# Performance work log

Measured on AMD Instinct MI355X. Metric: run time of the kernel, lower is better.

The kernel has to match this reference:

```python
import jax, jax.numpy as jnp
import numpy as np

D_MODEL = 2816
N_EXPERTS = 64
TOP_K = 8
RMS_EPS = 1e-6


def setup_inputs() -> dict:
    key = jax.random.key(0)
    k1, k2, k3, k4 = jax.random.split(key, 4)
    x = jax.random.normal(k1, (8, 4096, D_MODEL), dtype=jnp.float32)
    W = jax.random.normal(k2, (N_EXPERTS, D_MODEL), dtype=jnp.float32) * (D_MODEL ** -0.5)
    scale = jax.random.uniform(k3, (D_MODEL,), dtype=jnp.float32)
    per_expert_scale = jax.random.uniform(k4, (N_EXPERTS,), dtype=jnp.float32)
    return {"x": x, "W": W, "scale": scale, "per_expert_scale": per_expert_scale}


def reference(x, W, scale, per_expert_scale):
    # RMSNorm (no learned scale in norm itself)
    v = jnp.mean(jnp.square(x), axis=-1, keepdims=True)
    h = x * jax.lax.rsqrt(v + RMS_EPS)
    # elementwise scale + 1/sqrt(d)
    h = h * scale * (D_MODEL ** -0.5)
    # tiny projection to expert logits: [B,S,E]
    scores = jnp.einsum('bsd,ed->bse', h, W)
    prob = jax.nn.softmax(scores, axis=-1)
    topw, topi = jax.lax.top_k(prob, TOP_K)          # [B,S,K]
    topw = topw / jnp.sum(topw, axis=-1, keepdims=True)
    topw = topw * per_expert_scale[topi]
    # one-hot scatter back to dense [B,S,E]
    oh = jax.nn.one_hot(topi, N_EXPERTS, dtype=topw.dtype)  # [B,S,K,E]
    return jnp.einsum('bsk,bske->bse', topw, oh)
```

## Files before the change

kernel.cpp:

```cpp
#include <hip/hip_runtime.h>
#include <math.h>

#define D_MODEL 2816
#define N_EXP   64
#define TOPK    8
#define T_TILE  64
#define DC      32
#define NCHUNK  88
#define SROW    34
#define SMEM_BYTES 35072


__global__ __launch_bounds__(256, 2)
void router_fused(const float* __restrict__ x,
                  const float* __restrict__ W,
                  const float* __restrict__ scale,
                  const float* __restrict__ pes,
                  float* __restrict__ out)
{
    __shared__ __align__(16) char smem[SMEM_BYTES];
    double (*xs)[SROW] = (double (*)[SROW])(smem);
    double (*ws)[SROW] = (double (*)[SROW])(smem + 64 * SROW * 8);
    double* raw  = (double*)smem;
    float*  ssqp = (float*)(smem + 32768);
    float*  rn   = (float*)(smem + 34816);

    const int tid  = threadIdx.x;
    const int tb   = blockIdx.x * T_TILE;
    const int lrow = tid >> 3;
    const int kk   = tid & 7;
    const int tg4  = (tid >> 4) << 2;
    const int eg   = tid & 15;

    double acc[4][4] = {};
    float ssq2[2] = {0.f, 0.f};

    for (int c = 0; c < NCHUNK; ++c) {
        const int d0 = c * DC;
        float4 xg[2], wg[2];
        const float4 sc4 = *(const float4*)(scale + d0 + kk * 4);
        #pragma unroll
        for (int r = 0; r < 2; ++r) {
            const int row = r * 32 + lrow;
            xg[r] = *(const float4*)(x + (size_t)(tb + row) * D_MODEL + d0 + kk * 4);
            wg[r] = *(const float4*)(W + (size_t)row * D_MODEL + d0 + kk * 4);
        }
        __syncthreads();
        #pragma unroll
        for (int r = 0; r < 2; ++r) {
            const int row = r * 32 + lrow;
            ssq2[r] += xg[r].x * xg[r].x + xg[r].y * xg[r].y
                     + xg[r].z * xg[r].z + xg[r].w * xg[r].w;
            double2* xrow = (double2*)&xs[row][kk * 4];
            xrow[0] = make_double2((double)xg[r].x, (double)xg[r].y);
            xrow[1] = make_double2((double)xg[r].z, (double)xg[r].w);
            double2* wrow = (double2*)&ws[row][kk * 4];
            wrow[0] = make_double2((double)wg[r].x * (double)sc4.x,
                                   (double)wg[r].y * (double)sc4.y);
            wrow[1] = make_double2((double)wg[r].z * (double)sc4.z,
                                   (double)wg[r].w * (double)sc4.w);
        }
        __syncthreads();
        #pragma unroll 2
        for (int d = 0; d < DC; d += 2) {
            double2 xf[4], wf[4];
            #pragma unroll
            for (int u = 0; u < 4; ++u)
                xf[u] = *(const double2*)&xs[tg4 + u][d];
            #pragma unroll
            for (int v = 0; v < 4; ++v)
                wf[v] = *(const double2*)&ws[eg + 16 * v][d];
            #pragma unroll
            for (int u = 0; u < 4; ++u)
                #pragma unroll
                for (int v = 0; v < 4; ++v) {
                    acc[u][v] = fma(xf[u].x, wf[v].x, acc[u][v]);
                    acc[u][v] = fma(xf[u].y, wf[v].y, acc[u][v]);
                }
        }
    }

    __syncthreads();

    #pragma unroll
    for (int u = 0; u < 4; ++u)
        #pragma unroll
        for (int v = 0; v < 4; ++v)
            raw[(tg4 + u) * 64 + (eg + 16 * v)] = acc[u][v];
    ssqp[lrow * 8 + kk]        = ssq2[0];
    ssqp[(32 + lrow) * 8 + kk] = ssq2[1];
    __syncthreads();

    if (tid < 64) {
        float s = 0.f;
        #pragma unroll
        for (int j = 0; j < 8; ++j) s += ssqp[tid * 8 + j];
        float v  = s + 0.002816f;
        float r0 = rsqrtf(v);
        r0 = r0 * (1.5f - 0.5f * v * r0 * r0);
        rn[tid] = r0;
    }
    __syncthreads();

    const int wv = tid >> 6, lane = tid & 63;
    const float pl = pes[lane];
    for (int tk = 0; tk < 16; ++tk) {
        const int t = wv * 16 + tk;
        const double sraw = raw[t * 64 + lane];
        double m = sraw;
        #pragma unroll
        for (int off = 32; off > 0; off >>= 1) {
            double o = __shfl_xor(m, off);
            m = m > o ? m : o;
        }
        int rank = 0;
        for (int j = 0; j < 64; ++j) {
            double sj = raw[t * 64 + j];
            rank += (sj > sraw) || (sj == sraw && j < lane);
        }
        const bool sel = rank < TOPK;
        const float rt = rn[t];
        float ex = sel ? __expf((float)(sraw - m) * rt) : 0.f;
        float sum = ex;
        #pragma unroll
        for (int off = 32; off > 0; off >>= 1) sum += __shfl_xor(sum, off);
        out[(size_t)(tb + t) * N_EXP + lane] = sel ? (ex / sum) * pl : 0.f;
    }
}

extern "C" void kernel_launch(void* const* d_in, const int* in_sizes, int n_in,
                              void* d_out, int out_size, void* d_ws, size_t ws_size,
                              hipStream_t stream) {
    const float* x     = (const float*)d_in[0];
    const float* W     = (const float*)d_in[1];
    const float* scale = (const float*)d_in[2];
    const float* pes   = (const float*)d_in[3];
    float* out = (float*)d_out;

    const int ntok    = in_sizes[0] / D_MODEL;
    const int nblocks = ntok / T_TILE;
    router_fused<<<dim3(nblocks), dim3(256), 0, stream>>>(x, W, scale, pes, out);
}
```

Before: 729.1 us.

## Compute router logits in fp32 with fp64 recompute for ambiguous top-k tokens

Moves the main logit GEMM from fp64 to fp32 with float4 shared-memory tiles and halves shared memory. Tokens whose top-k boundary gap falls below a tolerance are appended to a global list with an atomic counter. A second kernel recomputes those tokens in fp64 and overwrites their outputs. The aim is to drop costly fp64 FMA throughput while keeping top-k selection exact, at the cost of an extra memset, a second launch, and a correctness dependence on the tolerance.

```diff
diff --git a/kernel.cpp b/kernel.cpp
--- a/kernel.cpp
+++ b/kernel.cpp
@@ -1,5 +1,6 @@
 #include <hip/hip_runtime.h>
 #include <math.h>
+#include <float.h>
 
 #define D_MODEL 2816
 #define N_EXP   64
@@ -7,23 +8,27 @@
 #define T_TILE  64
 #define DC      32
 #define NCHUNK  88
-#define SROW    34
-#define SMEM_BYTES 35072
+#define SROW    36
+#define SMEM_BYTES 18688
+#define TAU     3e-4f
 
 
 __global__ __launch_bounds__(256, 2)
-void router_fused(const float* __restrict__ x,
-                  const float* __restrict__ W,
-                  const float* __restrict__ scale,
-                  const float* __restrict__ pes,
-                  float* __restrict__ out)
+void router_a(const float* __restrict__ x,
+              const float* __restrict__ W,
+              const float* __restrict__ scale,
+              const float* __restrict__ pes,
+              float* __restrict__ out,
+              unsigned int* __restrict__ cnt,
+              int* __restrict__ list,
+              int cap)
 {
     __shared__ __align__(16) char smem[SMEM_BYTES];
-    double (*xs)[SROW] = (double (*)[SROW])(smem);
-    double (*ws)[SROW] = (double (*)[SROW])(smem + 64 * SROW * 8);
-    double* raw  = (double*)smem;
-    float*  ssqp = (float*)(smem + 32768);
-    float*  rn   = (float*)(smem + 34816);
+    float (*xs)[SROW] = (float (*)[SROW])(smem);
+    float (*ws)[SROW] = (float (*)[SROW])(smem + 9216);
+    float* raw  = (float*)smem;
+    float* ssqp = (float*)(smem + 16384);
+    float* rn   = (float*)(smem + 18432);
 
     const int tid  = threadIdx.x;
     const int tb   = blockIdx.x * T_TILE;
@@ -32,7 +37,7 @@
     const int tg4  = (tid >> 4) << 2;
     const int eg   = tid & 15;
 
-    double acc[4][4] = {};
+    float acc[4][4] = {};
     float ssq2[2] = {0.f, 0.f};
 
     for (int c = 0; c < NCHUNK; ++c) {
@@ -51,31 +56,30 @@
             const int row = r * 32 + lrow;
             ssq2[r] += xg[r].x * xg[r].x + xg[r].y * xg[r].y
                      + xg[r].z * xg[r].z + xg[r].w * xg[r].w;
-            double2* xrow = (double2*)&xs[row][kk * 4];
-            xrow[0] = make_double2((double)xg[r].x, (double)xg[r].y);
-            xrow[1] = make_double2((double)xg[r].z, (double)xg[r].w);
-            double2* wrow = (double2*)&ws[row][kk * 4];
-            wrow[0] = make_double2((double)wg[r].x * (double)sc4.x,
-                                   (double)wg[r].y * (double)sc4.y);
-            wrow[1] = make_double2((double)wg[r].z * (double)sc4.z,
-                                   (double)wg[r].w * (double)sc4.w);
-        }
-        __syncthreads();
-        #pragma unroll 2
-        for (int d = 0; d < DC; d += 2) {
-            double2 xf[4], wf[4];
+            *(float4*)&xs[row][kk * 4] = xg[r];
+            float4 wv;
+            wv.x = wg[r].x * sc4.x; wv.y = wg[r].y * sc4.y;
+            wv.z = wg[r].z * sc4.z; wv.w = wg[r].w * sc4.w;
+            *(float4*)&ws[row][kk * 4] = wv;
+        }
+        __syncthreads();
+        #pragma unroll
+        for (int d = 0; d < DC; d += 4) {
+            float4 xf[4], wf[4];
             #pragma unroll
             for (int u = 0; u < 4; ++u)
-                xf[u] = *(const double2*)&xs[tg4 + u][d];
+                xf[u] = *(const float4*)&xs[tg4 + u][d];
             #pragma unroll
             for (int v = 0; v < 4; ++v)
-                wf[v] = *(const double2*)&ws[eg + 16 * v][d];
+                wf[v] = *(const float4*)&ws[eg + 16 * v][d];
             #pragma unroll
             for (int u = 0; u < 4; ++u)
                 #pragma unroll
                 for (int v = 0; v < 4; ++v) {
-                    acc[u][v] = fma(xf[u].x, wf[v].x, acc[u][v]);
-                    acc[u][v] = fma(xf[u].y, wf[v].y, acc[u][v]);
+                    acc[u][v] = fmaf(xf[u].x, wf[v].x, acc[u][v]);
+                    acc[u][v] = fmaf(xf[u].y, wf[v].y, acc[u][v]);
+                    acc[u][v] = fmaf(xf[u].z, wf[v].z, acc[u][v]);
+                    acc[u][v] = fmaf(xf[u].w, wf[v].w, acc[u][v]);
                 }
         }
     }
@@ -106,25 +110,105 @@
     const float pl = pes[lane];
     for (int tk = 0; tk < 16; ++tk) {
         const int t = wv * 16 + tk;
-        const double sraw = raw[t * 64 + lane];
-        double m = sraw;
-        #pragma unroll
-        for (int off = 32; off > 0; off >>= 1) {
-            double o = __shfl_xor(m, off);
-            m = m > o ? m : o;
-        }
+        const float sraw = raw[t * 64 + lane];
+        float m = sraw;
         int rank = 0;
         for (int j = 0; j < 64; ++j) {
-            double sj = raw[t * 64 + j];
+            float sj = raw[t * 64 + j];
             rank += (sj > sraw) || (sj == sraw && j < lane);
         }
         const bool sel = rank < TOPK;
+        float a = sel ?  sraw :  FLT_MAX;
+        float b = sel ? -FLT_MAX :  sraw;
+        #pragma unroll
+        for (int off = 32; off > 0; off >>= 1) {
+            m = fmaxf(m, __shfl_xor(m, off));
+            a = fminf(a, __shfl_xor(a, off));
+            b = fmaxf(b, __shfl_xor(b, off));
+        }
         const float rt = rn[t];
-        float ex = sel ? __expf((float)(sraw - m) * rt) : 0.f;
+        float ex = sel ? __expf((sraw - m) * rt) : 0.f;
         float sum = ex;
         #pragma unroll
         for (int off = 32; off > 0; off >>= 1) sum += __shfl_xor(sum, off);
         out[(size_t)(tb + t) * N_EXP + lane] = sel ? (ex / sum) * pl : 0.f;
+        if (lane == 0 && (a - b) < TAU) {
+            unsigned int slot = atomicAdd(cnt, 1u);
+            if ((int)slot < cap) list[slot] = tb + t;
+        }
+    }
+}
+
+__global__ __launch_bounds__(256, 2)
+void router_b(const float* __restrict__ x,
+              const float* __restrict__ W,
+              const float* __restrict__ scale,
+              const float* __restrict__ pes,
+              float* __restrict__ out,
+              const unsigned int* __restrict__ cnt,
+              const int* __restrict__ list,
+              int cap)
+{
+    __shared__ double part[256];
+    __shared__ double sc[64];
+    __shared__ double qsh[4];
+
+    const int tid = threadIdx.x;
+    const int e   = tid & 63;
+    const int seg = tid >> 6;
+    int n = (int)*cnt;
+    if (n > cap) n = cap;
+
+    for (int i = blockIdx.x; i < n; i += gridDim.x) {
+        const int t = list[i];
+        const float* xr = x + (size_t)t * D_MODEL;
+        const float* wr = W + (size_t)e * D_MODEL;
+        double s = 0.0, q = 0.0;
+        const int dbeg = seg * 704;
+        for (int d = dbeg; d < dbeg + 704; d += 4) {
+            float4 xv = *(const float4*)(xr + d);
+            float4 wvv = *(const float4*)(wr + d);
+            float4 sv = *(const float4*)(scale + d);
+            s += (double)xv.x * ((double)sv.x * (double)wvv.x)
+               + (double)xv.y * ((double)sv.y * (double)wvv.y)
+               + (double)xv.z * ((double)sv.z * (double)wvv.z)
+               + (double)xv.w * ((double)sv.w * (double)wvv.w);
+            if (e == 0)
+                q += (double)xv.x * xv.x + (double)xv.y * xv.y
+                   + (double)xv.z * xv.z + (double)xv.w * xv.w;
+        }
+        part[tid] = s;
+        if (e == 0) qsh[seg] = q;
+        __syncthreads();
+        if (tid < 64)
+            sc[tid] = part[tid] + part[tid + 64] + part[tid + 128] + part[tid + 192];
+        __syncthreads();
+        if (tid < 64) {
+            const int lane = tid;
+            const double sraw = sc[lane];
+            double m = sraw;
+            #pragma unroll
+            for (int off = 32; off > 0; off >>= 1) {
+                double o = __shfl_xor(m, off);
+                m = m > o ? m : o;
+            }
+            int rank = 0;
+            for (int j = 0; j < 64; ++j) {
+                double sj = sc[j];
+                rank += (sj > sraw) || (sj == sraw && j < lane);
+            }
+            const bool sel = rank < TOPK;
+            float ssqf = (float)(qsh[0] + qsh[1] + qsh[2] + qsh[3]);
+            float v  = ssqf + 0.002816f;
+            float r0 = rsqrtf(v);
+            r0 = r0 * (1.5f - 0.5f * v * r0 * r0);
+            float ex = sel ? __expf((float)(sraw - m) * r0) : 0.f;
+            float sum = ex;
+            #pragma unroll
+            for (int off = 32; off > 0; off >>= 1) sum += __shfl_xor(sum, off);
+            out[(size_t)t * N_EXP + lane] = sel ? (ex / sum) * pes[lane] : 0.f;
+        }
+        __syncthreads();
     }
 }
 
@@ -137,7 +221,15 @@
     const float* pes   = (const float*)d_in[3];
     float* out = (float*)d_out;
 
+    unsigned int* cnt = (unsigned int*)d_ws;
+    int* list = (int*)((char*)d_ws + 16);
+    long cap_l = ((long)ws_size - 16) / 4;
+    int cap = cap_l < 0 ? 0 : (cap_l > 32768 ? 32768 : (int)cap_l);
+
     const int ntok    = in_sizes[0] / D_MODEL;
     const int nblocks = ntok / T_TILE;
-    router_fused<<<dim3(nblocks), dim3(256), 0, stream>>>(x, W, scale, pes, out);
+
+    hipMemsetAsync(d_ws, 0, 16, stream);
+    router_a<<<dim3(nblocks), dim3(256), 0, stream>>>(x, W, scale, pes, out, cnt, list, cap);
+    router_b<<<dim3(128), dim3(256), 0, stream>>>(x, W, scale, pes, out, cnt, list, cap);
 }
```

Result: no change. 736.3 us (+1.0%).
